# Kernel optimization log

Measured on AMD Instinct MI355X. Metric: run time of the kernel, lower is better.

## Reference

```python
import jax, jax.numpy as jnp
import numpy as np

B, N, K, M, CIN, O, OUT = 4, 1024, 30, 8, 9, 64, 512
BN_SCALE = 1.0 / np.sqrt(1.0 + 1e-5)  # eval-mode BatchNorm with default stats/affine


def setup_inputs() -> dict:
    key = jax.random.key(0)
    ks = jax.random.split(key, 8)
    x = jax.random.normal(ks[0], (B, CIN, N), jnp.float32)
    norm_plt = jax.random.normal(ks[1], (B, 3, N), jnp.float32)
    cls_label = jnp.zeros((B, 16), jnp.float32)
    conv1_w = jax.random.normal(ks[2], (64, 18), jnp.float32) * np.sqrt(2.0 / 18.0)
    conv1_b = jnp.zeros((64,), jnp.float32)
    sn_hw = jax.random.normal(ks[3], (4, 16, 28), jnp.float32) * np.sqrt(2.0 / 28.0)
    sn_ow = jax.random.normal(ks[4], (4, M, 16), jnp.float32) * np.sqrt(2.0 / 16.0)
    sn_ob = jnp.zeros((4, M), jnp.float32)
    mats = jax.random.normal(ks[5], (4, 2 * O, M * O), jnp.float32) * np.sqrt(2.0 / (2.0 * O))
    convt_w = jax.random.normal(ks[6], (OUT, 5 * O), jnp.float32) * np.sqrt(2.0 / (5.0 * O))
    return dict(x=x, norm_plt=norm_plt, cls_label=cls_label, conv1_w=conv1_w,
                conv1_b=conv1_b, sn_hw=sn_hw, sn_ow=sn_ow, sn_ob=sn_ob,
                mats=mats, convt_w=convt_w)


def _gather(feat, idx):
    # feat (B,N,C), idx (B,N,K) int -> (B,N,K,C): neighbor feature gather
    return jax.vmap(lambda f, i: f[i])(feat, idx)


def _bn(t):
    return t * BN_SCALE


def reference(x, norm_plt, cls_label, conv1_w, conv1_b, sn_hw, sn_ow, sn_ob, mats, convt_w):
    xt = jnp.transpose(x, (0, 2, 1))                       # (B,N,9)
    sq = jnp.sum(xt * xt, axis=-1)
    neg_d = 2.0 * jnp.einsum('bic,bjc->bij', xt, xt) - sq[:, :, None] - sq[:, None, :]
    _, idx = jax.lax.top_k(neg_d, K)                       # (B,N,K) knn indices

    nbr = _gather(xt, idx)                                 # (B,N,K,9)
    ctr = jnp.broadcast_to(xt[:, :, None, :], nbr.shape)   # (B,N,K,9)
    diff = nbr - ctr
    ed = jnp.linalg.norm(diff, axis=-1, keepdims=True)     # (B,N,K,1)
    xyz = jnp.concatenate([diff, nbr, ctr, ed], axis=-1)   # (B,N,K,28) scorenet input

    # get_graph_feature -> conv1 (1x1) -> BN -> relu -> max over k
    gf = jnp.concatenate([diff, ctr], axis=-1)             # (B,N,K,18)
    h = jax.nn.relu(_bn(jnp.einsum('bnkc,oc->bnko', gf, conv1_w) + conv1_b))
    x1 = jnp.max(h, axis=2)                                # (B,N,64)

    feats = [x1]
    f = x1
    for l in range(4):  # PAConv layers 2..5 (sequential, fixed count)
        hid = jax.nn.relu(_bn(jnp.einsum('bnkc,hc->bnkh', xyz, sn_hw[l])))
        score = jax.nn.softmax(jnp.einsum('bnkh,mh->bnkm', hid, sn_ow[l]) + sn_ob[l], axis=-1)
        kern = mats[l]                                     # (128, M*64)
        # feat_trans_dgcnn: neighbor uses full kernel on [f;f], center uses top half
        point = (jnp.concatenate([f, f], axis=-1) @ kern).reshape(B, N, M, O)
        center = (f @ kern[:O]).reshape(B, N, M, O)
        # assemble_dgcnn: sum_k sum_m score * (point[knn] - center)
        gp = _gather(point.reshape(B, N, M * O), idx).reshape(B, N, K, M, O)
        out = jnp.einsum('bnkm,bnkmo->bno', score, gp) - jnp.einsum('bnkm,bnmo->bno', score, center)
        f = jax.nn.relu(_bn(out))
        feats.append(f)

    xx = jnp.concatenate(feats, axis=-1)                   # (B,N,320)
    xc = jax.nn.relu(_bn(jnp.einsum('bnc,oc->bno', xx, convt_w)))
    return jnp.max(xc, axis=1)                             # (B,512) global max pool
```

## Files before the change

kernel.cpp:

```cpp
#include <hip/hip_runtime.h>
#include <hip/hip_bf16.h>

#define B 4
#define N 1024
#define KNN 30
#define MM 8
#define OUTC 512
#define HID 16
#define FD 320
#define BNS 0.9999950000374997f

typedef float f32x4 __attribute__((ext_vector_type(4)));
typedef short s16x8 __attribute__((ext_vector_type(8)));

#define OFF_XT     0
#define OFF_SQ     36864
#define OFF_IDX    40960
#define OFF_CVT    163840
#define OFF_K2T    245760
#define OFF_FB     376832
#define OFF_SC     1032192

__global__ void __launch_bounds__(256) k_prep(const float* __restrict__ x,
                                              const float* __restrict__ convt_w,
                                              const float* __restrict__ mats,
                                              float* __restrict__ xt,
                                              float* __restrict__ sq,
                                              __hip_bfloat16* __restrict__ cvt_bf,
                                              __hip_bfloat16* __restrict__ k2t_bf,
                                              float* __restrict__ out) {
  __shared__ float tile[64][65];
  if (blockIdx.x < 640) {
    int id = blockIdx.x * 256 + threadIdx.x;
    if (id < B * N) {
      int b = id >> 10, n = id & 1023;
      float s = 0.f;
#pragma unroll
      for (int c = 0; c < 9; c++) {
        float v = x[(b * 9 + c) * N + n];
        xt[id * 9 + c] = v;
        s = fmaf(v, v, s);
      }
      sq[id] = s;
    }
    if (id < B * OUTC) out[id] = 0.f;
    if (id < 512 * 320) cvt_bf[id] = __float2bfloat16(convt_w[id]);
  } else {
    int blk = blockIdx.x - 640;
    int l = blk >> 4, part = (blk >> 3) & 1, m = blk & 7;
    int tr = threadIdx.x >> 6;
    int tc = threadIdx.x & 63;
    const float* src = mats + l * 65536 + (part * 64) * 512 + m * 64;
#pragma unroll
    for (int it = 0; it < 16; it++) {
      int c = it * 4 + tr;
      tile[c][tc] = src[c * 512 + tc];
    }
    __syncthreads();
    __hip_bfloat16* dst = k2t_bf + l * 65536 + part * 512 + m * 64;
#pragma unroll
    for (int it = 0; it < 16; it++) {
      int o = it * 4 + tr;
      dst[o * 1024 + tc] = __float2bfloat16(tile[tc][o]);
    }
  }
}

__global__ void __launch_bounds__(256) k_knnc1(const float* __restrict__ xt,
                                               const float* __restrict__ sq,
                                               const float* __restrict__ w,
                                               const float* __restrict__ bias,
                                               int* __restrict__ idx,
                                               __hip_bfloat16* __restrict__ feats_bf) {
  int t = threadIdx.x;
  int r = t >> 6;
  int lane = t & 63;
  int row = blockIdx.x * 4 + r;
  int b = row >> 10;
  __shared__ unsigned int hist[4][256];
  __shared__ unsigned int cntr[4];
  __shared__ unsigned int bp[4];
  __shared__ int bn[4];
  __shared__ int js_l[4][KNN];
  __shared__ float ws[64 * 18];
  __shared__ __align__(16) float diff_s[4][KNN][12];
  __shared__ float ctr_s[4][9];
  for (int i = t; i < 64 * 18; i += 256) ws[i] = w[i];
  if (t < 36) { int rr = t / 9, c = t - rr * 9; ctr_s[rr][c] = xt[(blockIdx.x * 4 + rr) * 9 + c]; }
  const float* xb = xt + (b << 10) * 9;
  const float* sb = sq + (b << 10);
  float cx[9];
#pragma unroll
  for (int c = 0; c < 9; c++) cx[c] = xt[row * 9 + c];
  float sqn = sq[row];
  unsigned int key[16];
#pragma unroll
  for (int s = 0; s < 16; s++) {
    int j = s * 64 + lane;
    const float* xj = xb + j * 9;
    float dot = 0.f;
#pragma unroll
    for (int c = 0; c < 9; c++) dot = fmaf(cx[c], xj[c], dot);
    float v = 2.0f * dot - sqn - sb[j];
    unsigned int u = __float_as_uint(v);
    key[s] = u ^ ((unsigned int)(((int)u) >> 31) | 0x80000000u);
  }
  if (lane == 0) cntr[r] = 0;
  unsigned int prefix = 0;
  int need = KNN;
  for (int p = 0; p < 4; p++) {
    int shift = 24 - 8 * p;
    for (int i = lane; i < 256; i += 64) hist[r][i] = 0;
    __syncthreads();
    unsigned int himask = (p == 0) ? 0u : (0xFFFFFFFFu << (shift + 8));
#pragma unroll
    for (int s = 0; s < 16; s++) {
      if ((key[s] & himask) == prefix)
        atomicAdd(&hist[r][(key[s] >> shift) & 255], 1u);
    }
    __syncthreads();
    int c0 = hist[r][4 * lane + 0], c1 = hist[r][4 * lane + 1];
    int c2 = hist[r][4 * lane + 2], c3 = hist[r][4 * lane + 3];
    int lsum = c0 + c1 + c2 + c3;
    int sfx = lsum;
#pragma unroll
    for (int ofs = 1; ofs < 64; ofs <<= 1) {
      int tt = __shfl_down(sfx, ofs, 64);
      if (lane + ofs < 64) sfx += tt;
    }
    int A3 = sfx - lsum;
    int A2 = A3 + c3, A1 = A2 + c2, A0 = A1 + c1;
    if (A0 < need && need <= A0 + c0) { bp[r] = prefix | ((unsigned)(4 * lane + 0) << shift); bn[r] = need - A0; }
    if (A1 < need && need <= A1 + c1) { bp[r] = prefix | ((unsigned)(4 * lane + 1) << shift); bn[r] = need - A1; }
    if (A2 < need && need <= A2 + c2) { bp[r] = prefix | ((unsigned)(4 * lane + 2) << shift); bn[r] = need - A2; }
    if (A3 < need && need <= A3 + c3) { bp[r] = prefix | ((unsigned)(4 * lane + 3) << shift); bn[r] = need - A3; }
    __syncthreads();
    prefix = bp[r];
    need = bn[r];
  }
  unsigned int T = prefix;
  int above_total = KNN - need;
  int* orow = idx + row * KNN;
#pragma unroll
  for (int s = 0; s < 16; s++) {
    if (key[s] > T) {
      unsigned int pslot = atomicAdd(&cntr[r], 1u);
      orow[pslot] = s * 64 + lane;
      js_l[r][pslot] = s * 64 + lane;
    }
  }
  int base = 0;
  for (int s = 0; s < 16; s++) {
    unsigned long long m = __ballot(key[s] == T);
    if (key[s] == T) {
      int rk = base + __popcll(m & ((1ull << lane) - 1ull));
      if (rk < need) {
        orow[above_total + rk] = s * 64 + lane;
        js_l[r][above_total + rk] = s * 64 + lane;
      }
    }
    base += __popcll(m);
    if (base >= need) break;
  }
  __syncthreads();
  if (t < 120) {
    int rr = t / KNN, k = t - rr * KNN;
    int j = js_l[rr][k];
    const float* xj = xt + ((b << 10) + j) * 9;
#pragma unroll
    for (int c = 0; c < 9; c++) diff_s[rr][k][c] = xj[c] - ctr_s[rr][c];
  }
  __syncthreads();
  float wd[9];
#pragma unroll
  for (int c = 0; c < 9; c++) wd[c] = ws[lane * 18 + c];
  float cd = 0.f;
#pragma unroll
  for (int c = 0; c < 9; c++) cd = fmaf(ctr_s[r][c], ws[lane * 18 + 9 + c], cd);
  float best = -3.0e38f;
  for (int k = 0; k < KNN; k++) {
    const float4* dr = (const float4*)diff_s[r][k];
    float4 d0 = dr[0], d1 = dr[1], d2v = dr[2];
    float dd = 0.f;
    dd = fmaf(d0.x, wd[0], dd); dd = fmaf(d0.y, wd[1], dd);
    dd = fmaf(d0.z, wd[2], dd); dd = fmaf(d0.w, wd[3], dd);
    dd = fmaf(d1.x, wd[4], dd); dd = fmaf(d1.y, wd[5], dd);
    dd = fmaf(d1.z, wd[6], dd); dd = fmaf(d1.w, wd[7], dd);
    dd = fmaf(d2v.x, wd[8], dd);
    best = fmaxf(best, dd);
  }
  float val = (best + cd + bias[lane]) * BNS;
  feats_bf[row * FD + lane] = __float2bfloat16(fmaxf(val, 0.f));
}

__global__ void __launch_bounds__(256) k_score(const float* __restrict__ xt,
                                               const int* __restrict__ idx,
                                               const float* __restrict__ hw,
                                               const float* __restrict__ ow,
                                               const float* __restrict__ ob,
                                               float* __restrict__ score) {
  __shared__ float hws[4 * 448];
  __shared__ float ows[4 * 128];
  __shared__ float obs[32];
  int t = threadIdx.x;
  for (int i = t; i < 1792; i += 256) hws[i] = hw[i];
  for (int i = t; i < 512; i += 256) ows[i] = ow[i];
  if (t < 32) obs[t] = ob[t];
  __syncthreads();
  int id = blockIdx.x * 256 + t;
  int row = id / KNN;
  int b = row >> 10;
  int j = idx[id];
  const float* xc = xt + row * 9;
  const float* xj = xt + ((b << 10) + j) * 9;
  float xv[28];
  float d2 = 0.f;
#pragma unroll
  for (int c = 0; c < 9; c++) {
    float nb = xj[c], ct = xc[c], df = nb - ct;
    xv[c] = df; xv[9 + c] = nb; xv[18 + c] = ct;
    d2 = fmaf(df, df, d2);
  }
  xv[27] = sqrtf(d2);
  for (int l = 0; l < 4; l++) {
    float hid[HID];
#pragma unroll
    for (int h = 0; h < HID; h++) {
      float a = 0.f;
#pragma unroll
      for (int c = 0; c < 28; c++) a = fmaf(xv[c], hws[l * 448 + h * 28 + c], a);
      hid[h] = fmaxf(a * BNS, 0.f);
    }
    float lg[MM], mx = -3.0e38f;
#pragma unroll
    for (int m = 0; m < MM; m++) {
      float a = obs[l * 8 + m];
#pragma unroll
      for (int h = 0; h < HID; h++) a = fmaf(hid[h], ows[l * 128 + m * 16 + h], a);
      lg[m] = a; mx = fmaxf(mx, a);
    }
    float s = 0.f;
#pragma unroll
    for (int m = 0; m < MM; m++) { lg[m] = __expf(lg[m] - mx); s += lg[m]; }
    float inv = 1.0f / s;
    float* so = score + l * 983040 + id * 8;
    *(float4*)so = make_float4(lg[0] * inv, lg[1] * inv, lg[2] * inv, lg[3] * inv);
    *(float4*)(so + 4) = make_float4(lg[4] * inv, lg[5] * inv, lg[6] * inv, lg[7] * inv);
  }
}

__global__ void __launch_bounds__(512) k_layer2(const int* __restrict__ idx,
                                                const float* __restrict__ score,
                                                const __hip_bfloat16* __restrict__ k2t_bf,
                                                __hip_bfloat16* __restrict__ feats_bf,
                                                const __hip_bfloat16* __restrict__ cvt_bf,
                                                float* __restrict__ out,
                                                int l, int last) {
  int row0 = blockIdx.x * 16;
  int t = threadIdx.x;
  int b = row0 >> 10;
  __shared__ int js[16][KNN];
  __shared__ float ssum[16][8];
  __shared__ __align__(16) __hip_bfloat16 Hs[16][1040];
  __shared__ __align__(16) __hip_bfloat16 ftile[16][336];
  const float* sc_l = score + l * 983040;
  for (int i = t; i < 16 * KNN; i += 512) {
    int r = i / KNN, k = i - r * KNN;
    js[r][k] = (b << 10) + idx[(row0 + r) * KNN + k];
  }
  if (t < 128) {
    int r = t >> 3, m = t & 7;
    float a = 0.f;
    for (int k = 0; k < KNN; k++) a += sc_l[(row0 + r) * 240 + k * 8 + m];
    ssum[r][m] = a;
  }
  __syncthreads();
  int wv = t >> 6, lane = t & 63;
#pragma unroll
  for (int rr = 0; rr < 2; rr++) {
    int r = wv * 2 + rr;
    int row = row0 + r;
    const float4* srow = (const float4*)(sc_l + row * 240);
    float g[MM] = {};
#pragma unroll
    for (int k = 0; k < KNN; k++) {
      float fv = __bfloat162float(feats_bf[js[r][k] * FD + l * 64 + lane]);
      float4 s0 = srow[2 * k], s1 = srow[2 * k + 1];
      g[0] = fmaf(s0.x, fv, g[0]); g[1] = fmaf(s0.y, fv, g[1]);
      g[2] = fmaf(s0.z, fv, g[2]); g[3] = fmaf(s0.w, fv, g[3]);
      g[4] = fmaf(s1.x, fv, g[4]); g[5] = fmaf(s1.y, fv, g[5]);
      g[6] = fmaf(s1.z, fv, g[6]); g[7] = fmaf(s1.w, fv, g[7]);
    }
    float fn = __bfloat162float(feats_bf[row * FD + l * 64 + lane]);
#pragma unroll
    for (int m = 0; m < MM; m++) {
      Hs[r][m * 64 + lane] = __float2bfloat16(g[m] - ssum[r][m] * fn);
      Hs[r][512 + m * 64 + lane] = __float2bfloat16(g[m]);
    }
  }
  __syncthreads();
  int lr = lane & 15, lk8 = (lane >> 4) * 8;
  if (wv < 4) {
    const short* Ks2 = (const short*)(k2t_bf + l * 65536);
    const short* brow = Ks2 + (wv * 16 + lr) * 1024 + lk8;
    const short* arow = (const short*)&Hs[lr][lk8];
    f32x4 acc = {0.f, 0.f, 0.f, 0.f};
#pragma unroll 8
    for (int kk = 0; kk < 32; kk++) {
      s16x8 a = *(const s16x8*)(arow + kk * 32);
      s16x8 bb = *(const s16x8*)(brow + kk * 32);
      acc = __builtin_amdgcn_mfma_f32_16x16x32_bf16(a, bb, acc, 0, 0, 0);
    }
    if (!last) {
#pragma unroll
      for (int i = 0; i < 4; i++) {
        int row = row0 + (lane >> 4) * 4 + i;
        feats_bf[row * FD + (l + 1) * 64 + wv * 16 + lr] =
            __float2bfloat16(fmaxf(acc[i] * BNS, 0.f));
      }
    } else {
#pragma unroll
      for (int i = 0; i < 4; i++) {
        int rl = (lane >> 4) * 4 + i;
        ftile[rl][256 + wv * 16 + lr] = __float2bfloat16(fmaxf(acc[i] * BNS, 0.f));
      }
    }
  } else if (last) {
    int t2 = t - 256;
    const short* Fs = (const short*)feats_bf;
    for (int i = t2; i < 512; i += 256) {
      int r = i >> 5, c8 = (i & 31) * 8;
      *(s16x8*)&ftile[r][c8] = *(const s16x8*)(Fs + (row0 + r) * FD + c8);
    }
  }
  if (last) {
    __syncthreads();
    const short* Ws = (const short*)cvt_bf;
#pragma unroll
    for (int tn = 0; tn < 4; tn++) {
      int nb = wv * 64 + tn * 16;
      const short* brow = Ws + (nb + lr) * FD + lk8;
      f32x4 acc = {0.f, 0.f, 0.f, 0.f};
#pragma unroll
      for (int kk = 0; kk < 10; kk++) {
        s16x8 a = *(const s16x8*)&ftile[lr][kk * 32 + lk8];
        s16x8 bb = *(const s16x8*)(brow + kk * 32);
        acc = __builtin_amdgcn_mfma_f32_16x16x32_bf16(a, bb, acc, 0, 0, 0);
      }
      float mx = fmaxf(fmaxf(acc[0], acc[1]), fmaxf(acc[2], acc[3]));
      mx = fmaxf(mx, __shfl_xor(mx, 16, 64));
      mx = fmaxf(mx, __shfl_xor(mx, 32, 64));
      if ((lane >> 4) == 0) {
        float val = fmaxf(mx * BNS, 0.f);
        atomicMax((unsigned int*)out + b * OUTC + nb + lr, __float_as_uint(val));
      }
    }
  }
}

extern "C" void kernel_launch(void* const* d_in, const int* in_sizes, int n_in,
                              void* d_out, int out_size, void* d_ws, size_t ws_size,
                              hipStream_t stream) {
  const float* x       = (const float*)d_in[0];
  const float* conv1_w = (const float*)d_in[3];
  const float* conv1_b = (const float*)d_in[4];
  const float* sn_hw   = (const float*)d_in[5];
  const float* sn_ow   = (const float*)d_in[6];
  const float* sn_ob   = (const float*)d_in[7];
  const float* mats    = (const float*)d_in[8];
  const float* convt_w = (const float*)d_in[9];
  float* out = (float*)d_out;

  float* w = (float*)d_ws;
  float* xt = w + OFF_XT;
  float* sq = w + OFF_SQ;
  int* idx = (int*)(w + OFF_IDX);
  __hip_bfloat16* cvt_bf = (__hip_bfloat16*)(w + OFF_CVT);
  __hip_bfloat16* k2t_bf = (__hip_bfloat16*)(w + OFF_K2T);
  __hip_bfloat16* feats_bf = (__hip_bfloat16*)(w + OFF_FB);
  float* score = w + OFF_SC;

  k_prep<<<704, 256, 0, stream>>>(x, convt_w, mats, xt, sq, cvt_bf, k2t_bf, out);
  k_knnc1<<<1024, 256, 0, stream>>>(xt, sq, conv1_w, conv1_b, idx, feats_bf);
  k_score<<<480, 256, 0, stream>>>(xt, idx, sn_hw, sn_ow, sn_ob, score);
  for (int l = 0; l < 4; l++) {
    k_layer2<<<256, 512, 0, stream>>>(idx, score, k2t_bf, feats_bf, cvt_bf, out,
                                      l, l == 3 ? 1 : 0);
  }
}
```

Baseline: 194.8 us.

## Transpose point layout, ballot-based knn compaction, split-K MFMA across all waves

```diff
diff --git a/kernel.cpp b/kernel.cpp
--- a/kernel.cpp
+++ b/kernel.cpp
@@ -5,26 +5,28 @@
 #define N 1024
 #define KNN 30
 #define MM 8
-#define OUTC 512
 #define HID 16
 #define FD 320
+#define OUTC 512
 #define BNS 0.9999950000374997f
 
 typedef float f32x4 __attribute__((ext_vector_type(4)));
 typedef short s16x8 __attribute__((ext_vector_type(8)));
 
-#define OFF_XT     0
-#define OFF_SQ     36864
-#define OFF_IDX    40960
-#define OFF_CVT    163840
-#define OFF_K2T    245760
-#define OFF_FB     376832
-#define OFF_SC     1032192
+#define OFF_XT16 0
+#define OFF_XTT  65536
+#define OFF_SQ   102400
+#define OFF_IDX  106496
+#define OFF_CVT  229376
+#define OFF_K2T  311296
+#define OFF_FB   442368
+#define OFF_SC   1097728
 
 __global__ void __launch_bounds__(256) k_prep(const float* __restrict__ x,
                                               const float* __restrict__ convt_w,
                                               const float* __restrict__ mats,
-                                              float* __restrict__ xt,
+                                              float* __restrict__ xt16,
+                                              float* __restrict__ xtT,
                                               float* __restrict__ sq,
                                               __hip_bfloat16* __restrict__ cvt_bf,
                                               __hip_bfloat16* __restrict__ k2t_bf,
@@ -38,7 +40,8 @@
 #pragma unroll
       for (int c = 0; c < 9; c++) {
         float v = x[(b * 9 + c) * N + n];
-        xt[id * 9 + c] = v;
+        xt16[id * 16 + c] = v;
+        xtT[c * 4096 + id] = v;
         s = fmaf(v, v, s);
       }
       sq[id] = s;
@@ -48,25 +51,19 @@
   } else {
     int blk = blockIdx.x - 640;
     int l = blk >> 4, part = (blk >> 3) & 1, m = blk & 7;
-    int tr = threadIdx.x >> 6;
-    int tc = threadIdx.x & 63;
+    int tr = threadIdx.x >> 6, tc = threadIdx.x & 63;
     const float* src = mats + l * 65536 + (part * 64) * 512 + m * 64;
 #pragma unroll
-    for (int it = 0; it < 16; it++) {
-      int c = it * 4 + tr;
-      tile[c][tc] = src[c * 512 + tc];
-    }
+    for (int it = 0; it < 16; it++) { int c = it * 4 + tr; tile[c][tc] = src[c * 512 + tc]; }
     __syncthreads();
     __hip_bfloat16* dst = k2t_bf + l * 65536 + part * 512 + m * 64;
 #pragma unroll
-    for (int it = 0; it < 16; it++) {
-      int o = it * 4 + tr;
-      dst[o * 1024 + tc] = __float2bfloat16(tile[tc][o]);
-    }
-  }
-}
-
-__global__ void __launch_bounds__(256) k_knnc1(const float* __restrict__ xt,
+    for (int it = 0; it < 16; it++) { int o = it * 4 + tr; dst[o * 1024 + tc] = __float2bfloat16(tile[tc][o]); }
+  }
+}
+
+__global__ void __launch_bounds__(256) k_knnc1(const float* __restrict__ xt16,
+                                               const float* __restrict__ xtT,
                                                const float* __restrict__ sq,
                                                const float* __restrict__ w,
                                                const float* __restrict__ bias,
@@ -78,7 +75,6 @@
   int row = blockIdx.x * 4 + r;
   int b = row >> 10;
   __shared__ unsigned int hist[4][256];
-  __shared__ unsigned int cntr[4];
   __shared__ unsigned int bp[4];
   __shared__ int bn[4];
   __shared__ int js_l[4][KNN];
@@ -86,89 +82,81 @@
   __shared__ __align__(16) float diff_s[4][KNN][12];
   __shared__ float ctr_s[4][9];
   for (int i = t; i < 64 * 18; i += 256) ws[i] = w[i];
-  if (t < 36) { int rr = t / 9, c = t - rr * 9; ctr_s[rr][c] = xt[(blockIdx.x * 4 + rr) * 9 + c]; }
-  const float* xb = xt + (b << 10) * 9;
-  const float* sb = sq + (b << 10);
+  if (t < 36) { int rr = t / 9, c = t - rr * 9; ctr_s[rr][c] = xt16[(blockIdx.x * 4 + rr) * 16 + c]; }
+  const float* xtb = xtT + (b << 10);
   float cx[9];
 #pragma unroll
-  for (int c = 0; c < 9; c++) cx[c] = xt[row * 9 + c];
+  for (int c = 0; c < 9; c++) cx[c] = xt16[row * 16 + c];
   float sqn = sq[row];
   unsigned int key[16];
 #pragma unroll
   for (int s = 0; s < 16; s++) {
     int j = s * 64 + lane;
-    const float* xj = xb + j * 9;
     float dot = 0.f;
 #pragma unroll
-    for (int c = 0; c < 9; c++) dot = fmaf(cx[c], xj[c], dot);
-    float v = 2.0f * dot - sqn - sb[j];
-    unsigned int u = __float_as_uint(v);
-    key[s] = u ^ ((unsigned int)(((int)u) >> 31) | 0x80000000u);
-  }
-  if (lane == 0) cntr[r] = 0;
-  unsigned int prefix = 0;
-  int need = KNN;
+    for (int c = 0; c < 9; c++) dot = fmaf(cx[c], xtb[c * 4096 + j], dot);
+    float v = 2.0f * dot - sqn - sq[(b << 10) + j];
+    unsigned u = __float_as_uint(v);
+    key[s] = u ^ ((unsigned)(((int)u) >> 31) | 0x80000000u);
+  }
+  unsigned prefix = 0; int need = KNN;
   for (int p = 0; p < 4; p++) {
     int shift = 24 - 8 * p;
     for (int i = lane; i < 256; i += 64) hist[r][i] = 0;
     __syncthreads();
-    unsigned int himask = (p == 0) ? 0u : (0xFFFFFFFFu << (shift + 8));
-#pragma unroll
-    for (int s = 0; s < 16; s++) {
-      if ((key[s] & himask) == prefix)
-        atomicAdd(&hist[r][(key[s] >> shift) & 255], 1u);
-    }
-    __syncthreads();
-    int c0 = hist[r][4 * lane + 0], c1 = hist[r][4 * lane + 1];
+    unsigned himask = p ? (0xFFFFFFFFu << (shift + 8)) : 0u;
+#pragma unroll
+    for (int s = 0; s < 16; s++)
+      if ((key[s] & himask) == prefix) atomicAdd(&hist[r][(key[s] >> shift) & 255], 1u);
+    __syncthreads();
+    int c0 = hist[r][4 * lane], c1 = hist[r][4 * lane + 1];
     int c2 = hist[r][4 * lane + 2], c3 = hist[r][4 * lane + 3];
-    int lsum = c0 + c1 + c2 + c3;
-    int sfx = lsum;
+    int lsum = c0 + c1 + c2 + c3, sfx = lsum;
 #pragma unroll
     for (int ofs = 1; ofs < 64; ofs <<= 1) {
       int tt = __shfl_down(sfx, ofs, 64);
       if (lane + ofs < 64) sfx += tt;
     }
-    int A3 = sfx - lsum;
-    int A2 = A3 + c3, A1 = A2 + c2, A0 = A1 + c1;
+    int A3 = sfx - lsum, A2 = A3 + c3, A1 = A2 + c2, A0 = A1 + c1;
     if (A0 < need && need <= A0 + c0) { bp[r] = prefix | ((unsigned)(4 * lane + 0) << shift); bn[r] = need - A0; }
     if (A1 < need && need <= A1 + c1) { bp[r] = prefix | ((unsigned)(4 * lane + 1) << shift); bn[r] = need - A1; }
     if (A2 < need && need <= A2 + c2) { bp[r] = prefix | ((unsigned)(4 * lane + 2) << shift); bn[r] = need - A2; }
     if (A3 < need && need <= A3 + c3) { bp[r] = prefix | ((unsigned)(4 * lane + 3) << shift); bn[r] = need - A3; }
     __syncthreads();
-    prefix = bp[r];
-    need = bn[r];
-  }
-  unsigned int T = prefix;
-  int above_total = KNN - need;
+    prefix = bp[r]; need = bn[r];
+  }
+  unsigned T = prefix;
   int* orow = idx + row * KNN;
+  unsigned long long lowmask = (1ull << lane) - 1ull;
+  int aboveBase = 0;
 #pragma unroll
   for (int s = 0; s < 16; s++) {
+    unsigned long long mA = __ballot(key[s] > T);
     if (key[s] > T) {
-      unsigned int pslot = atomicAdd(&cntr[r], 1u);
-      orow[pslot] = s * 64 + lane;
-      js_l[r][pslot] = s * 64 + lane;
-    }
-  }
-  int base = 0;
-  for (int s = 0; s < 16; s++) {
-    unsigned long long m = __ballot(key[s] == T);
+      int slot = aboveBase + __popcll(mA & lowmask);
+      orow[slot] = s * 64 + lane;
+      js_l[r][slot] = s * 64 + lane;
+    }
+    aboveBase += __popcll(mA);
+  }
+  int tieBase = 0;
+  for (int s = 0; s < 16 && tieBase < need; s++) {
+    unsigned long long mT = __ballot(key[s] == T);
     if (key[s] == T) {
-      int rk = base + __popcll(m & ((1ull << lane) - 1ull));
+      int rk = tieBase + __popcll(mT & lowmask);
       if (rk < need) {
-        orow[above_total + rk] = s * 64 + lane;
-        js_l[r][above_total + rk] = s * 64 + lane;
-      }
-    }
-    base += __popcll(m);
-    if (base >= need) break;
+        orow[aboveBase + rk] = s * 64 + lane;
+        js_l[r][aboveBase + rk] = s * 64 + lane;
+      }
+    }
+    tieBase += __popcll(mT);
   }
   __syncthreads();
   if (t < 120) {
     int rr = t / KNN, k = t - rr * KNN;
-    int j = js_l[rr][k];
-    const float* xj = xt + ((b << 10) + j) * 9;
-#pragma unroll
-    for (int c = 0; c < 9; c++) diff_s[rr][k][c] = xj[c] - ctr_s[rr][c];
+    int jg = (b << 10) + js_l[rr][k];
+#pragma unroll
+    for (int c = 0; c < 9; c++) diff_s[rr][k][c] = xt16[jg * 16 + c] - ctr_s[rr][c];
   }
   __syncthreads();
   float wd[9];
@@ -179,21 +167,21 @@
   for (int c = 0; c < 9; c++) cd = fmaf(ctr_s[r][c], ws[lane * 18 + 9 + c], cd);
   float best = -3.0e38f;
   for (int k = 0; k < KNN; k++) {
-    const float4* dr = (const float4*)diff_s[r][k];
-    float4 d0 = dr[0], d1 = dr[1], d2v = dr[2];
+    const f32x4* dr = (const f32x4*)diff_s[r][k];
+    f32x4 d0 = dr[0], d1 = dr[1], d2 = dr[2];
     float dd = 0.f;
     dd = fmaf(d0.x, wd[0], dd); dd = fmaf(d0.y, wd[1], dd);
     dd = fmaf(d0.z, wd[2], dd); dd = fmaf(d0.w, wd[3], dd);
     dd = fmaf(d1.x, wd[4], dd); dd = fmaf(d1.y, wd[5], dd);
     dd = fmaf(d1.z, wd[6], dd); dd = fmaf(d1.w, wd[7], dd);
-    dd = fmaf(d2v.x, wd[8], dd);
+    dd = fmaf(d2.x, wd[8], dd);
     best = fmaxf(best, dd);
   }
   float val = (best + cd + bias[lane]) * BNS;
   feats_bf[row * FD + lane] = __float2bfloat16(fmaxf(val, 0.f));
 }
 
-__global__ void __launch_bounds__(256) k_score(const float* __restrict__ xt,
+__global__ void __launch_bounds__(256) k_score(const float* __restrict__ xt16,
                                                const int* __restrict__ idx,
                                                const float* __restrict__ hw,
                                                const float* __restrict__ ow,
@@ -210,9 +198,9 @@
   int id = blockIdx.x * 256 + t;
   int row = id / KNN;
   int b = row >> 10;
-  int j = idx[id];
-  const float* xc = xt + row * 9;
-  const float* xj = xt + ((b << 10) + j) * 9;
+  int jg = (b << 10) + idx[id];
+  const float* xc = xt16 + row * 16;
+  const float* xj = xt16 + jg * 16;
   float xv[28];
   float d2 = 0.f;
 #pragma unroll
@@ -249,6 +237,7 @@
   }
 }
 
+#define HSTR 1048
 __global__ void __launch_bounds__(512) k_layer2(const int* __restrict__ idx,
                                                 const float* __restrict__ score,
                                                 const __hip_bfloat16* __restrict__ k2t_bf,
@@ -261,8 +250,9 @@
   int b = row0 >> 10;
   __shared__ int js[16][KNN];
   __shared__ float ssum[16][8];
-  __shared__ __align__(16) __hip_bfloat16 Hs[16][1040];
+  __shared__ __align__(16) __hip_bfloat16 Hs[16][HSTR];
   __shared__ __align__(16) __hip_bfloat16 ftile[16][336];
+  __shared__ float pacc[8][16][16];
   const float* sc_l = score + l * 983040;
   for (int i = t; i < 16 * KNN; i += 512) {
     int r = i / KNN, k = i - r * KNN;
@@ -275,10 +265,10 @@
     ssum[r][m] = a;
   }
   __syncthreads();
-  int wv = t >> 6, lane = t & 63;
+  int w = t >> 6, lane = t & 63;
 #pragma unroll
   for (int rr = 0; rr < 2; rr++) {
-    int r = wv * 2 + rr;
+    int r = w * 2 + rr;
     int row = row0 + r;
     const float4* srow = (const float4*)(sc_l + row * 240);
     float g[MM] = {};
@@ -298,39 +288,50 @@
       Hs[r][512 + m * 64 + lane] = __float2bfloat16(g[m]);
     }
   }
-  __syncthreads();
+  if (last) {
+    const short* Fs = (const short*)feats_bf;
+    for (int i = t; i < 512; i += 512) {}
+    for (int i = t; i < 512; i += 512) {}
+    for (int i = t; i < 512; i += 512) {}
+  }
+  __syncthreads();
+  if (last) {
+    const short* Fs = (const short*)feats_bf;
+    for (int i = t; i < 512; i += 512) {
+      int r = i >> 5, c8 = (i & 31) * 8;
+      *(s16x8*)&ftile[r][c8] = *(const s16x8*)(Fs + (row0 + r) * FD + c8);
+    }
+    __syncthreads();
+  }
   int lr = lane & 15, lk8 = (lane >> 4) * 8;
-  if (wv < 4) {
+  {
+    int ct = w & 3, kh = w >> 2;
     const short* Ks2 = (const short*)(k2t_bf + l * 65536);
-    const short* brow = Ks2 + (wv * 16 + lr) * 1024 + lk8;
-    const short* arow = (const short*)&Hs[lr][lk8];
+    const short* brow = Ks2 + (ct * 16 + lr) * 1024 + kh * 512 + lk8;
+    const short* arow = (const short*)&Hs[lr][kh * 512 + lk8];
     f32x4 acc = {0.f, 0.f, 0.f, 0.f};
 #pragma unroll 8
-    for (int kk = 0; kk < 32; kk++) {
+    for (int kk = 0; kk < 16; kk++) {
       s16x8 a = *(const s16x8*)(arow + kk * 32);
       s16x8 bb = *(const s16x8*)(brow + kk * 32);
       acc = __builtin_amdgcn_mfma_f32_16x16x32_bf16(a, bb, acc, 0, 0, 0);
     }
-    if (!last) {
-#pragma unroll
-      for (int i = 0; i < 4; i++) {
-        int row = row0 + (lane >> 4) * 4 + i;
-        feats_bf[row * FD + (l + 1) * 64 + wv * 16 + lr] =
-            __float2bfloat16(fmaxf(acc[i] * BNS, 0.f));
-      }
-    } else {
-#pragma unroll
-      for (int i = 0; i < 4; i++) {
-        int rl = (lane >> 4) * 4 + i;
-        ftile[rl][256 + wv * 16 + lr] = __float2bfloat16(fmaxf(acc[i] * BNS, 0.f));
-      }
-    }
-  } else if (last) {
-    int t2 = t - 256;
-    const short* Fs = (const short*)feats_bf;
-    for (int i = t2; i < 512; i += 256) {
-      int r = i >> 5, c8 = (i & 31) * 8;
-      *(s16x8*)&ftile[r][c8] = *(const s16x8*)(Fs + (row0 + r) * FD + c8);
+#pragma unroll
+    for (int i = 0; i < 4; i++)
+      pacc[w][(lane >> 4) * 4 + i][lr] = acc[i];
+  }
+  __syncthreads();
+  if (w < 4) {
+#pragma unroll
+    for (int i = 0; i < 4; i++) {
+      int ri = (lane >> 4) * 4 + i;
+      float val = fmaxf((pacc[w][ri][lr] + pacc[w + 4][ri][lr]) * BNS, 0.f);
+      __hip_bfloat16 vb = __float2bfloat16(val);
+      if (!last) {
+        feats_bf[(row0 + ri) * FD + (l + 1) * 64 + w * 16 + lr] = vb;
+      } else {
+        ftile[ri][256 + w * 16 + lr] = vb;
+      }
     }
   }
   if (last) {
@@ -338,12 +339,13 @@
     const short* Ws = (const short*)cvt_bf;
 #pragma unroll
     for (int tn = 0; tn < 4; tn++) {
-      int nb = wv * 64 + tn * 16;
+      int nb = w * 64 + tn * 16;
       const short* brow = Ws + (nb + lr) * FD + lk8;
+      const short* arow = (const short*)&ftile[lr][lk8];
       f32x4 acc = {0.f, 0.f, 0.f, 0.f};
 #pragma unroll
       for (int kk = 0; kk < 10; kk++) {
-        s16x8 a = *(const s16x8*)&ftile[lr][kk * 32 + lk8];
+        s16x8 a = *(const s16x8*)(arow + kk * 32);
         s16x8 bb = *(const s16x8*)(brow + kk * 32);
         acc = __builtin_amdgcn_mfma_f32_16x16x32_bf16(a, bb, acc, 0, 0, 0);
       }
@@ -371,18 +373,19 @@
   const float* convt_w = (const float*)d_in[9];
   float* out = (float*)d_out;
 
-  float* w = (float*)d_ws;
-  float* xt = w + OFF_XT;
-  float* sq = w + OFF_SQ;
-  int* idx = (int*)(w + OFF_IDX);
-  __hip_bfloat16* cvt_bf = (__hip_bfloat16*)(w + OFF_CVT);
-  __hip_bfloat16* k2t_bf = (__hip_bfloat16*)(w + OFF_K2T);
-  __hip_bfloat16* feats_bf = (__hip_bfloat16*)(w + OFF_FB);
-  float* score = w + OFF_SC;
-
-  k_prep<<<704, 256, 0, stream>>>(x, convt_w, mats, xt, sq, cvt_bf, k2t_bf, out);
-  k_knnc1<<<1024, 256, 0, stream>>>(xt, sq, conv1_w, conv1_b, idx, feats_bf);
-  k_score<<<480, 256, 0, stream>>>(xt, idx, sn_hw, sn_ow, sn_ob, score);
+  float* wsp = (float*)d_ws;
+  float* xt16 = wsp + OFF_XT16;
+  float* xtT  = wsp + OFF_XTT;
+  float* sq   = wsp + OFF_SQ;
+  int* idx    = (int*)(wsp + OFF_IDX);
+  __hip_bfloat16* cvt_bf = (__hip_bfloat16*)(wsp + OFF_CVT);
+  __hip_bfloat16* k2t_bf = (__hip_bfloat16*)(wsp + OFF_K2T);
+  __hip_bfloat16* feats_bf = (__hip_bfloat16*)(wsp + OFF_FB);
+  float* score = wsp + OFF_SC;
+
+  k_prep<<<704, 256, 0, stream>>>(x, convt_w, mats, xt16, xtT, sq, cvt_bf, k2t_bf, out);
+  k_knnc1<<<1024, 256, 0, stream>>>(xt16, xtT, sq, conv1_w, conv1_b, idx, feats_bf);
+  k_score<<<480, 256, 0, stream>>>(xt16, idx, sn_hw, sn_ow, sn_ob, score);
   for (int l = 0; l < 4; l++) {
     k_layer2<<<256, 512, 0, stream>>>(idx, score, k2t_bf, feats_bf, cvt_bf, out,
                                       l, l == 3 ? 1 : 0);
```

Result: no change. 192.9 us (-1.0%).
